# Kernel tuning notes

Measured on AMD Instinct MI355X. Metric: run time of the kernel, lower is better.

The kernel has to match this reference:

```python
import jax, jax.numpy as jnp
import numpy as np

B, C, N, H = 4, 256, 4096, 4
DK = C // H


def _proj(x, w, b):
    # Conv1d with kernel size 1 == per-point linear: [B,C,N] x [O,C] -> [B,O,N]
    return jnp.einsum('oc,bcn->bon', w, x) + b[None, :, None]


def setup_inputs() -> dict:
    key = jax.random.key(0)
    ks = jax.random.split(key, 9)
    s = 1.0 / np.sqrt(C)
    return {
        'x': jax.random.normal(ks[0], (B, C, N), jnp.float32),
        'wq': jax.random.normal(ks[1], (C, C), jnp.float32) * s,
        'bq': jax.random.normal(ks[2], (C,), jnp.float32) * 0.01,
        'wk': jax.random.normal(ks[3], (C, C), jnp.float32) * s,
        'bk': jax.random.normal(ks[4], (C,), jnp.float32) * 0.01,
        'wv': jax.random.normal(ks[5], (C, C), jnp.float32) * s,
        'bv': jax.random.normal(ks[6], (C,), jnp.float32) * 0.01,
        'wp': jax.random.normal(ks[7], (C, C), jnp.float32) * s,
        'bp': jax.random.normal(ks[8], (C,), jnp.float32) * 0.01,
    }


def reference(x, wq, bq, wk, bk, wv, bv, wp, bp):
    b, c, n = x.shape
    q = _proj(x, wq, bq).reshape(b, H, DK, n)
    k = _proj(x, wk, bk).reshape(b, H, DK, n)
    v = _proj(x, wv, bv).reshape(b, H, DK, n)
    scale = 1.0 / jnp.sqrt(jnp.asarray(DK, x.dtype))
    # scores over point pairs: [B,H,N,N]
    scores = jnp.einsum('bhdn,bhdm->bhnm', q, k) * scale
    attn = jax.nn.softmax(scores, axis=-1)
    out = jnp.einsum('bhnm,bhdm->bhdn', attn, v)  # [B,H,DK,N]
    out = out.reshape(b, c, n)
    out = _proj(out, wp, bp)
    return out + x
```

## Files before the change

kernel.cpp:

```cpp
#include <hip/hip_runtime.h>


#define BDIM 4
#define CDIM 256
#define NDIM 4096
#define HDIM 4
#define DKDIM 64
#define QSCALE 0.18033688011112042f

typedef __bf16 bf16x8 __attribute__((ext_vector_type(8)));
typedef float f32x4 __attribute__((ext_vector_type(4)));
typedef short s16x4 __attribute__((ext_vector_type(4)));
typedef unsigned short u16;

__device__ __forceinline__ u16 f2bf(float f) {
  union { __bf16 h; u16 s; } u; u.h = (__bf16)f; return u.s;
}

__global__ __launch_bounds__(256) void wcvt_kernel(
    const float* __restrict__ w0, const float* __restrict__ w1,
    const float* __restrict__ w2, const float* __restrict__ w3,
    u16* __restrict__ d0, u16* __restrict__ d1,
    u16* __restrict__ d2, u16* __restrict__ d3)
{
  const int row = blockIdx.x;
  const int m = blockIdx.y;
  const float* s = (m == 0) ? w0 : (m == 1) ? w1 : (m == 2) ? w2 : w3;
  u16* d = (m == 0) ? d0 : (m == 1) ? d1 : (m == 2) ? d2 : d3;
  const float sc = (m == 0) ? QSCALE : 1.0f;
  const int idx = row * CDIM + threadIdx.x;
  d[idx] = f2bf(s[idx] * sc);
}

__global__ __launch_bounds__(256) void xt_kernel(
    const float* __restrict__ x, u16* __restrict__ xT)
{
  const int b = blockIdx.z, c0 = blockIdx.y * 64, n0 = blockIdx.x * 64;
  __shared__ __align__(16) float T[64][68];
  const int t = threadIdx.x;
  {
    const int cr = t >> 4, nc = (t & 15) * 4;
    #pragma unroll
    for (int ci = 0; ci < 4; ++ci) {
      const float4 v = *(const float4*)&x[((size_t)(b * CDIM + c0 + cr + ci * 16)) * NDIM + n0 + nc];
      *(float4*)&T[cr + ci * 16][nc] = v;
    }
  }
  __syncthreads();
  {
    const int n = t >> 2, g = t & 3;
    union { u16 u[16]; uint4 v[2]; } pk;
    #pragma unroll
    for (int u_ = 0; u_ < 16; ++u_) pk.u[u_] = f2bf(T[g * 16 + u_][n]);
    uint4* dst = (uint4*)&xT[((size_t)(b * NDIM + n0 + n)) * CDIM + c0 + g * 16];
    dst[0] = pk.v[0]; dst[1] = pk.v[1];
  }
}

template<int MODE>
__global__ __launch_bounds__(256, 2) void proj_kernel(
    const u16* __restrict__ xT, const u16* __restrict__ wb,
    const float* __restrict__ bias, const float* __restrict__ res,
    void* __restrict__ outp, float bscale)
{
  const int b = blockIdx.z, o0 = blockIdx.y * 128, n0 = blockIdx.x * 64;
  __shared__ __align__(16) u16 XTs[64][40];
  __shared__ __align__(16) u16 Ws[128][40];
  const int t = threadIdx.x, lane = t & 63, w = t >> 6;
  const int qd = lane >> 4, lm = lane & 15;

  f32x4 acc[4][2];
  #pragma unroll
  for (int nt = 0; nt < 4; ++nt)
    #pragma unroll
    for (int j = 0; j < 2; ++j) acc[nt][j] = (f32x4){0.f, 0.f, 0.f, 0.f};

  for (int cs = 0; cs < 8; ++cs) {
    const int c0 = cs * 32;
    __syncthreads();
    {
      const int r = t >> 2, g = t & 3;
      *(uint4*)&XTs[r][g * 8] =
          *(const uint4*)&xT[((size_t)(b * NDIM + n0 + r)) * CDIM + c0 + g * 8];
      const int r2 = t >> 1, g2 = (t & 1) * 16;
      const u16* wr = &wb[(size_t)(o0 + r2) * CDIM + c0 + g2];
      *(uint4*)&Ws[r2][g2]     = *(const uint4*)(wr);
      *(uint4*)&Ws[r2][g2 + 8] = *(const uint4*)(wr + 8);
    }
    __syncthreads();
    bf16x8 xf[4], wf[2];
    #pragma unroll
    for (int nt = 0; nt < 4; ++nt) xf[nt] = *(const bf16x8*)&XTs[16 * nt + lm][qd * 8];
    #pragma unroll
    for (int j = 0; j < 2; ++j) wf[j] = *(const bf16x8*)&Ws[32 * w + 16 * j + lm][qd * 8];
    #pragma unroll
    for (int nt = 0; nt < 4; ++nt)
      #pragma unroll
      for (int j = 0; j < 2; ++j) {
        if constexpr (MODE == 0)
          acc[nt][j] = __builtin_amdgcn_mfma_f32_16x16x32_bf16(xf[nt], wf[j], acc[nt][j], 0, 0, 0);
        else
          acc[nt][j] = __builtin_amdgcn_mfma_f32_16x16x32_bf16(wf[j], xf[nt], acc[nt][j], 0, 0, 0);
      }
  }

  if constexpr (MODE == 0) {
    u16* out = (u16*)outp;
    #pragma unroll
    for (int j = 0; j < 2; ++j) {
      const int og = o0 + 32 * w + 16 * j + lm;
      const float bv = bias[og] * bscale;
      #pragma unroll
      for (int nt = 0; nt < 4; ++nt)
        #pragma unroll
        for (int r = 0; r < 4; ++r) {
          const int n = n0 + 16 * nt + 4 * qd + r;
          out[((size_t)(b * NDIM + n)) * CDIM + og] = f2bf(acc[nt][j][r] + bv);
        }
    }
  } else {
    #pragma unroll
    for (int j = 0; j < 2; ++j) {
      const float4 b4 = *(const float4*)&bias[o0 + 32 * w + 16 * j + 4 * qd];
      const float bvr[4] = {b4.x, b4.y, b4.z, b4.w};
      #pragma unroll
      for (int nt = 0; nt < 4; ++nt)
        #pragma unroll
        for (int r = 0; r < 4; ++r) {
          const int og = o0 + 32 * w + 16 * j + 4 * qd + r;
          const int n = n0 + 16 * nt + lm;
          const size_t idx = ((size_t)(b * CDIM + og)) * NDIM + n;
          const float val = acc[nt][j][r] + bvr[r];
          if constexpr (MODE == 1) ((u16*)outp)[idx] = f2bf(val);
          else ((float*)outp)[idx] = val + res[idx];
        }
    }
  }
}

__global__ __launch_bounds__(256, 2) void attn_kernel(
    const u16* __restrict__ qT, const u16* __restrict__ kT,
    const u16* __restrict__ vB, u16* __restrict__ abT)
{
  const int bh = blockIdx.y, b = bh >> 2, h = bh & 3;
  const int n0 = blockIdx.x * 128;
  __shared__ __align__(16) u16 Qt[128][72];
  __shared__ __align__(16) u16 Kt[64][72];
  __shared__ __align__(16) u16 Vt[64][72];

  const int t = threadIdx.x, lane = t & 63, w = t >> 6;
  const int qd = lane >> 4, lm = lane & 15;

  {
    const int r = t >> 1, g = (t & 1) * 32;
    const uint4* src = (const uint4*)&qT[((size_t)(b * NDIM + n0 + r)) * CDIM + h * 64 + g];
    uint4* dst = (uint4*)&Qt[r][g];
    dst[0] = src[0]; dst[1] = src[1]; dst[2] = src[2]; dst[3] = src[3];
  }
  __syncthreads();
  bf16x8 qf[2][2];
  #pragma unroll
  for (int s = 0; s < 2; ++s)
    #pragma unroll
    for (int hh = 0; hh < 2; ++hh)
      qf[s][hh] = *(const bf16x8*)&Qt[16 * (2 * w + s) + lm][32 * hh + qd * 8];

  float m_i[2] = {-1e30f, -1e30f}, l_i[2] = {0.f, 0.f};
  f32x4 oa[2][4];
  #pragma unroll
  for (int s = 0; s < 2; ++s)
    #pragma unroll
    for (int dt = 0; dt < 4; ++dt) oa[s][dt] = (f32x4){0.f, 0.f, 0.f, 0.f};

  for (int kt = 0; kt < NDIM; kt += 64) {
    __syncthreads();
    {
      const int r = t >> 2, g = (t & 3) * 16;
      const uint4* ks = (const uint4*)&kT[((size_t)(b * NDIM + kt + r)) * CDIM + h * 64 + g];
      uint4* kd = (uint4*)&Kt[r][g];
      kd[0] = ks[0]; kd[1] = ks[1];
      const uint4* vs = (const uint4*)&vB[((size_t)(b * CDIM + h * 64 + r)) * NDIM + kt + g];
      uint4* vd = (uint4*)&Vt[r][g];
      vd[0] = vs[0]; vd[1] = vs[1];
    }
    __syncthreads();

    bf16x8 kf[4][2];
    #pragma unroll
    for (int nt = 0; nt < 4; ++nt)
      #pragma unroll
      for (int hh = 0; hh < 2; ++hh)
        kf[nt][hh] = *(const bf16x8*)&Kt[16 * nt + lm][32 * hh + qd * 8];

    float pr[2][4][4];
    #pragma unroll
    for (int s = 0; s < 2; ++s) {
      f32x4 sc[4];
      #pragma unroll
      for (int nt = 0; nt < 4; ++nt) {
        f32x4 z = (f32x4){0.f, 0.f, 0.f, 0.f};
        z = __builtin_amdgcn_mfma_f32_16x16x32_bf16(kf[nt][0], qf[s][0], z, 0, 0, 0);
        z = __builtin_amdgcn_mfma_f32_16x16x32_bf16(kf[nt][1], qf[s][1], z, 0, 0, 0);
        sc[nt] = z;
      }
      float mx = sc[0][0];
      #pragma unroll
      for (int nt = 0; nt < 4; ++nt)
        #pragma unroll
        for (int r = 0; r < 4; ++r) mx = fmaxf(mx, sc[nt][r]);
      mx = fmaxf(mx, __shfl_xor(mx, 16));
      mx = fmaxf(mx, __shfl_xor(mx, 32));
      const float mn = fmaxf(m_i[s], mx);
      const float al = __builtin_amdgcn_exp2f(m_i[s] - mn);
      m_i[s] = mn;
      float rs = 0.f;
      #pragma unroll
      for (int nt = 0; nt < 4; ++nt)
        #pragma unroll
        for (int r = 0; r < 4; ++r) {
          const float p = __builtin_amdgcn_exp2f(sc[nt][r] - mn);
          pr[s][nt][r] = p;
          rs += p;
        }
      rs += __shfl_xor(rs, 16);
      rs += __shfl_xor(rs, 32);
      l_i[s] = l_i[s] * al + rs;
      #pragma unroll
      for (int dt = 0; dt < 4; ++dt) oa[s][dt] *= al;
    }

    #pragma unroll
    for (int c = 0; c < 4; ++c) {
      s16x4 av[4];
      #pragma unroll
      for (int dt = 0; dt < 4; ++dt)
        av[dt] = *(const s16x4*)&Vt[16 * dt + lm][16 * c + 4 * qd];
      union { u16 u[4]; s16x4 v; } bp0, bp1;
      #pragma unroll
      for (int r = 0; r < 4; ++r) { bp0.u[r] = f2bf(pr[0][c][r]); bp1.u[r] = f2bf(pr[1][c][r]); }
      #pragma unroll
      for (int dt = 0; dt < 4; ++dt) {
        oa[0][dt] = __builtin_amdgcn_mfma_f32_16x16x16bf16_1k(av[dt], bp0.v, oa[0][dt], 0, 0, 0);
        oa[1][dt] = __builtin_amdgcn_mfma_f32_16x16x16bf16_1k(av[dt], bp1.v, oa[1][dt], 0, 0, 0);
      }
    }
  }

  __syncthreads();
  u16 (*Ot)[72] = (u16(*)[72])&Qt[0][0];
  #pragma unroll
  for (int s = 0; s < 2; ++s) {
    const float inv = 1.0f / l_i[s];
    #pragma unroll
    for (int dt = 0; dt < 4; ++dt)
      #pragma unroll
      for (int r = 0; r < 4; ++r)
        Ot[16 * (2 * w + s) + lm][16 * dt + 4 * qd + r] = f2bf(oa[s][dt][r] * inv);
  }
  __syncthreads();
  {
    const int r = t >> 1, g = (t & 1) * 32;
    uint4* dst = (uint4*)&abT[((size_t)(b * NDIM + n0 + r)) * CDIM + h * 64 + g];
    const uint4* srcp = (const uint4*)&Ot[r][g];
    dst[0] = srcp[0]; dst[1] = srcp[1]; dst[2] = srcp[2]; dst[3] = srcp[3];
  }
}

extern "C" void kernel_launch(void* const* d_in, const int* in_sizes, int n_in,
                              void* d_out, int out_size, void* d_ws, size_t ws_size,
                              hipStream_t stream)
{
  const float* x  = (const float*)d_in[0];
  const float* wq = (const float*)d_in[1];
  const float* bq = (const float*)d_in[2];
  const float* wk = (const float*)d_in[3];
  const float* bk = (const float*)d_in[4];
  const float* wv = (const float*)d_in[5];
  const float* bv = (const float*)d_in[6];
  const float* wp = (const float*)d_in[7];
  const float* bp = (const float*)d_in[8];
  float* out = (float*)d_out;

  const size_t sz = (size_t)BDIM * CDIM * NDIM;
  const size_t wsz = (size_t)CDIM * CDIM;
  u16* xTb = (u16*)d_ws;
  u16* wqb = xTb + sz;
  u16* wkb = wqb + wsz;
  u16* wvb = wkb + wsz;
  u16* wpb = wvb + wsz;
  u16* qTb = wpb + wsz;
  u16* kTb = qTb + sz;
  u16* vBb = kTb + sz;
  u16* abT = vBb + sz;

  const dim3 blk(256);
  wcvt_kernel<<<dim3(CDIM, 4), blk, 0, stream>>>(wq, wk, wv, wp, wqb, wkb, wvb, wpb);
  xt_kernel<<<dim3(NDIM / 64, CDIM / 64, BDIM), blk, 0, stream>>>(x, xTb);
  const dim3 gp(NDIM / 64, 2, BDIM);
  proj_kernel<0><<<gp, blk, 0, stream>>>(xTb, wqb, bq, nullptr, qTb, QSCALE);
  proj_kernel<0><<<gp, blk, 0, stream>>>(xTb, wkb, bk, nullptr, kTb, 1.0f);
  proj_kernel<1><<<gp, blk, 0, stream>>>(xTb, wvb, bv, nullptr, vBb, 1.0f);
  attn_kernel<<<dim3(NDIM / 128, BDIM * HDIM), blk, 0, stream>>>(qTb, kTb, vBb, abT);
  proj_kernel<2><<<gp, blk, 0, stream>>>(abT, wpb, bp, x, out, 1.0f);
}
```

Before: 239.4 us.

## Split attention KV range in two with combine kernel, shrink projection tiles

The attention kernel now divides the key/value sequence into two halves across a third grid dimension. Each half writes a normalized partial output plus its row max and sum, and a new combine kernel merges the two with log-sum-exp weights. This doubles the number of attention blocks (512 → 1024) to fill more CUs, at the cost of extra partial-output traffic and one more launch. The running-max rescale is also skipped when no lane's max increases. Projection kernels use 64-wide output tiles with higher occupancy bounds, which doubles their grid.

```diff
diff --git a/kernel.cpp b/kernel.cpp
--- a/kernel.cpp
+++ b/kernel.cpp
@@ -6,6 +6,7 @@
 #define NDIM 4096
 #define HDIM 4
 #define DKDIM 64
+#define NQ   (BDIM * HDIM * NDIM)
 #define QSCALE 0.18033688011112042f
 
 typedef __bf16 bf16x8 __attribute__((ext_vector_type(8)));
@@ -15,6 +16,9 @@
 
 __device__ __forceinline__ u16 f2bf(float f) {
   union { __bf16 h; u16 s; } u; u.h = (__bf16)f; return u.s;
+}
+__device__ __forceinline__ float bf2f(u16 v) {
+  union { unsigned u; float f; } x; x.u = (unsigned)v << 16; return x.f;
 }
 
 __global__ __launch_bounds__(256) void wcvt_kernel(
@@ -58,92 +62,79 @@
 }
 
 template<int MODE>
-__global__ __launch_bounds__(256, 2) void proj_kernel(
+__global__ __launch_bounds__(256, 4) void proj_kernel(
     const u16* __restrict__ xT, const u16* __restrict__ wb,
     const float* __restrict__ bias, const float* __restrict__ res,
     void* __restrict__ outp, float bscale)
 {
-  const int b = blockIdx.z, o0 = blockIdx.y * 128, n0 = blockIdx.x * 64;
+  const int b = blockIdx.z, o0 = blockIdx.y * 64, n0 = blockIdx.x * 64;
   __shared__ __align__(16) u16 XTs[64][40];
-  __shared__ __align__(16) u16 Ws[128][40];
+  __shared__ __align__(16) u16 Ws[64][40];
   const int t = threadIdx.x, lane = t & 63, w = t >> 6;
   const int qd = lane >> 4, lm = lane & 15;
-
-  f32x4 acc[4][2];
-  #pragma unroll
-  for (int nt = 0; nt < 4; ++nt)
-    #pragma unroll
-    for (int j = 0; j < 2; ++j) acc[nt][j] = (f32x4){0.f, 0.f, 0.f, 0.f};
+  const int sr = t >> 2, sg = (t & 3) * 8;
+
+  const u16* xsrc = xT + ((size_t)(b * NDIM + n0 + sr)) * CDIM + sg;
+  const u16* wsrc = wb + ((size_t)(o0 + sr)) * CDIM + sg;
+
+  f32x4 acc[4];
+  #pragma unroll
+  for (int nt = 0; nt < 4; ++nt) acc[nt] = (f32x4){0.f, 0.f, 0.f, 0.f};
 
   for (int cs = 0; cs < 8; ++cs) {
-    const int c0 = cs * 32;
     __syncthreads();
-    {
-      const int r = t >> 2, g = t & 3;
-      *(uint4*)&XTs[r][g * 8] =
-          *(const uint4*)&xT[((size_t)(b * NDIM + n0 + r)) * CDIM + c0 + g * 8];
-      const int r2 = t >> 1, g2 = (t & 1) * 16;
-      const u16* wr = &wb[(size_t)(o0 + r2) * CDIM + c0 + g2];
-      *(uint4*)&Ws[r2][g2]     = *(const uint4*)(wr);
-      *(uint4*)&Ws[r2][g2 + 8] = *(const uint4*)(wr + 8);
-    }
+    *(uint4*)&XTs[sr][sg] = *(const uint4*)(xsrc + cs * 32);
+    *(uint4*)&Ws[sr][sg]  = *(const uint4*)(wsrc + cs * 32);
     __syncthreads();
-    bf16x8 xf[4], wf[2];
+    bf16x8 xf[4];
     #pragma unroll
     for (int nt = 0; nt < 4; ++nt) xf[nt] = *(const bf16x8*)&XTs[16 * nt + lm][qd * 8];
-    #pragma unroll
-    for (int j = 0; j < 2; ++j) wf[j] = *(const bf16x8*)&Ws[32 * w + 16 * j + lm][qd * 8];
-    #pragma unroll
-    for (int nt = 0; nt < 4; ++nt)
-      #pragma unroll
-      for (int j = 0; j < 2; ++j) {
-        if constexpr (MODE == 0)
-          acc[nt][j] = __builtin_amdgcn_mfma_f32_16x16x32_bf16(xf[nt], wf[j], acc[nt][j], 0, 0, 0);
-        else
-          acc[nt][j] = __builtin_amdgcn_mfma_f32_16x16x32_bf16(wf[j], xf[nt], acc[nt][j], 0, 0, 0);
-      }
+    const bf16x8 wf = *(const bf16x8*)&Ws[16 * w + lm][qd * 8];
+    #pragma unroll
+    for (int nt = 0; nt < 4; ++nt) {
+      if constexpr (MODE == 0)
+        acc[nt] = __builtin_amdgcn_mfma_f32_16x16x32_bf16(xf[nt], wf, acc[nt], 0, 0, 0);
+      else
+        acc[nt] = __builtin_amdgcn_mfma_f32_16x16x32_bf16(wf, xf[nt], acc[nt], 0, 0, 0);
+    }
   }
 
   if constexpr (MODE == 0) {
     u16* out = (u16*)outp;
-    #pragma unroll
-    for (int j = 0; j < 2; ++j) {
-      const int og = o0 + 32 * w + 16 * j + lm;
-      const float bv = bias[og] * bscale;
-      #pragma unroll
-      for (int nt = 0; nt < 4; ++nt)
-        #pragma unroll
-        for (int r = 0; r < 4; ++r) {
-          const int n = n0 + 16 * nt + 4 * qd + r;
-          out[((size_t)(b * NDIM + n)) * CDIM + og] = f2bf(acc[nt][j][r] + bv);
-        }
-    }
+    const int og = o0 + 16 * w + lm;
+    const float bv = bias[og] * bscale;
+    #pragma unroll
+    for (int nt = 0; nt < 4; ++nt)
+      #pragma unroll
+      for (int r = 0; r < 4; ++r) {
+        const int n = n0 + 16 * nt + 4 * qd + r;
+        out[((size_t)(b * NDIM + n)) * CDIM + og] = f2bf(acc[nt][r] + bv);
+      }
   } else {
-    #pragma unroll
-    for (int j = 0; j < 2; ++j) {
-      const float4 b4 = *(const float4*)&bias[o0 + 32 * w + 16 * j + 4 * qd];
-      const float bvr[4] = {b4.x, b4.y, b4.z, b4.w};
-      #pragma unroll
-      for (int nt = 0; nt < 4; ++nt)
-        #pragma unroll
-        for (int r = 0; r < 4; ++r) {
-          const int og = o0 + 32 * w + 16 * j + 4 * qd + r;
-          const int n = n0 + 16 * nt + lm;
-          const size_t idx = ((size_t)(b * CDIM + og)) * NDIM + n;
-          const float val = acc[nt][j][r] + bvr[r];
-          if constexpr (MODE == 1) ((u16*)outp)[idx] = f2bf(val);
-          else ((float*)outp)[idx] = val + res[idx];
-        }
-    }
-  }
-}
-
-__global__ __launch_bounds__(256, 2) void attn_kernel(
+    const float4 b4 = *(const float4*)&bias[o0 + 16 * w + 4 * qd];
+    const float bvr[4] = {b4.x, b4.y, b4.z, b4.w};
+    #pragma unroll
+    for (int nt = 0; nt < 4; ++nt)
+      #pragma unroll
+      for (int r = 0; r < 4; ++r) {
+        const int og = o0 + 16 * w + 4 * qd + r;
+        const int n = n0 + 16 * nt + lm;
+        const size_t idx = ((size_t)(b * CDIM + og)) * NDIM + n;
+        const float val = acc[nt][r] + bvr[r];
+        if constexpr (MODE == 1) ((u16*)outp)[idx] = f2bf(val);
+        else ((float*)outp)[idx] = val + res[idx];
+      }
+  }
+}
+
+__global__ __launch_bounds__(256, 4) void attn_kernel(
     const u16* __restrict__ qT, const u16* __restrict__ kT,
-    const u16* __restrict__ vB, u16* __restrict__ abT)
+    const u16* __restrict__ vB, u16* __restrict__ Opart,
+    float* __restrict__ Mp, float* __restrict__ Lp)
 {
   const int bh = blockIdx.y, b = bh >> 2, h = bh & 3;
   const int n0 = blockIdx.x * 128;
+  const int z  = blockIdx.z;
   __shared__ __align__(16) u16 Qt[128][72];
   __shared__ __align__(16) u16 Kt[64][72];
   __shared__ __align__(16) u16 Vt[64][72];
@@ -172,17 +163,22 @@
     #pragma unroll
     for (int dt = 0; dt < 4; ++dt) oa[s][dt] = (f32x4){0.f, 0.f, 0.f, 0.f};
 
-  for (int kt = 0; kt < NDIM; kt += 64) {
+  const int sr = t >> 2, sg = (t & 3) * 16;
+  const u16* kptr = kT + ((size_t)(b * NDIM) + z * 2048 + sr) * CDIM + h * 64 + sg;
+  const u16* vptr = vB + ((size_t)(b * CDIM) + h * 64 + sr) * NDIM + z * 2048 + sg;
+
+  for (int it = 0; it < 32; ++it) {
     __syncthreads();
     {
-      const int r = t >> 2, g = (t & 3) * 16;
-      const uint4* ks = (const uint4*)&kT[((size_t)(b * NDIM + kt + r)) * CDIM + h * 64 + g];
-      uint4* kd = (uint4*)&Kt[r][g];
-      kd[0] = ks[0]; kd[1] = ks[1];
-      const uint4* vs = (const uint4*)&vB[((size_t)(b * CDIM + h * 64 + r)) * NDIM + kt + g];
-      uint4* vd = (uint4*)&Vt[r][g];
-      vd[0] = vs[0]; vd[1] = vs[1];
-    }
+      uint4* kd = (uint4*)&Kt[sr][sg];
+      kd[0] = *(const uint4*)(kptr);
+      kd[1] = *(const uint4*)(kptr + 8);
+      uint4* vd = (uint4*)&Vt[sr][sg];
+      vd[0] = *(const uint4*)(vptr);
+      vd[1] = *(const uint4*)(vptr + 8);
+    }
+    kptr += (size_t)64 * CDIM;
+    vptr += 64;
     __syncthreads();
 
     bf16x8 kf[4][2];
@@ -198,10 +194,10 @@
       f32x4 sc[4];
       #pragma unroll
       for (int nt = 0; nt < 4; ++nt) {
-        f32x4 z = (f32x4){0.f, 0.f, 0.f, 0.f};
-        z = __builtin_amdgcn_mfma_f32_16x16x32_bf16(kf[nt][0], qf[s][0], z, 0, 0, 0);
-        z = __builtin_amdgcn_mfma_f32_16x16x32_bf16(kf[nt][1], qf[s][1], z, 0, 0, 0);
-        sc[nt] = z;
+        f32x4 zz = (f32x4){0.f, 0.f, 0.f, 0.f};
+        zz = __builtin_amdgcn_mfma_f32_16x16x32_bf16(kf[nt][0], qf[s][0], zz, 0, 0, 0);
+        zz = __builtin_amdgcn_mfma_f32_16x16x32_bf16(kf[nt][1], qf[s][1], zz, 0, 0, 0);
+        sc[nt] = zz;
       }
       float mx = sc[0][0];
       #pragma unroll
@@ -211,7 +207,12 @@
       mx = fmaxf(mx, __shfl_xor(mx, 16));
       mx = fmaxf(mx, __shfl_xor(mx, 32));
       const float mn = fmaxf(m_i[s], mx);
-      const float al = __builtin_amdgcn_exp2f(m_i[s] - mn);
+      if (__any(mx > m_i[s])) {
+        const float al = __builtin_amdgcn_exp2f(m_i[s] - mn);
+        l_i[s] *= al;
+        #pragma unroll
+        for (int dt = 0; dt < 4; ++dt) oa[s][dt] *= al;
+      }
       m_i[s] = mn;
       float rs = 0.f;
       #pragma unroll
@@ -224,9 +225,7 @@
         }
       rs += __shfl_xor(rs, 16);
       rs += __shfl_xor(rs, 32);
-      l_i[s] = l_i[s] * al + rs;
-      #pragma unroll
-      for (int dt = 0; dt < 4; ++dt) oa[s][dt] *= al;
+      l_i[s] += rs;
     }
 
     #pragma unroll
@@ -257,13 +256,53 @@
       for (int r = 0; r < 4; ++r)
         Ot[16 * (2 * w + s) + lm][16 * dt + 4 * qd + r] = f2bf(oa[s][dt][r] * inv);
   }
+  if (qd == 0) {
+    const size_t mlbase = ((size_t)z * (BDIM * HDIM) + bh) * NDIM;
+    #pragma unroll
+    for (int s = 0; s < 2; ++s) {
+      const int q = n0 + 16 * (2 * w + s) + lm;
+      Mp[mlbase + q] = m_i[s];
+      Lp[mlbase + q] = l_i[s];
+    }
+  }
   __syncthreads();
   {
     const int r = t >> 1, g = (t & 1) * 32;
-    uint4* dst = (uint4*)&abT[((size_t)(b * NDIM + n0 + r)) * CDIM + h * 64 + g];
+    u16* dst = Opart + (((size_t)z * (BDIM * HDIM) + bh) * NDIM + n0 + r) * DKDIM + g;
     const uint4* srcp = (const uint4*)&Ot[r][g];
-    dst[0] = srcp[0]; dst[1] = srcp[1]; dst[2] = srcp[2]; dst[3] = srcp[3];
-  }
+    uint4* d4 = (uint4*)dst;
+    d4[0] = srcp[0]; d4[1] = srcp[1]; d4[2] = srcp[2]; d4[3] = srcp[3];
+  }
+}
+
+__global__ __launch_bounds__(256) void combine_kernel(
+    const u16* __restrict__ Opart, const float* __restrict__ Mp,
+    const float* __restrict__ Lp, u16* __restrict__ abT)
+{
+  const int t = threadIdx.x;
+  const int gq = blockIdx.x * 64 + (t >> 2);
+  const int seg = (t & 3) * 16;
+  const float m0 = Mp[gq], l0 = Lp[gq];
+  const float m1 = Mp[NQ + gq], l1 = Lp[NQ + gq];
+  const float M = fmaxf(m0, m1);
+  const float d0 = l0 * __builtin_amdgcn_exp2f(m0 - M);
+  const float d1 = l1 * __builtin_amdgcn_exp2f(m1 - M);
+  const float inv = 1.0f / (d0 + d1);
+  const float w0 = d0 * inv, w1 = d1 * inv;
+
+  const u16* p0 = Opart + (size_t)gq * DKDIM + seg;
+  const u16* p1 = Opart + (size_t)NQ * DKDIM + (size_t)gq * DKDIM + seg;
+  union { u16 u[16]; uint4 v[2]; } a0, a1, ov;
+  a0.v[0] = ((const uint4*)p0)[0]; a0.v[1] = ((const uint4*)p0)[1];
+  a1.v[0] = ((const uint4*)p1)[0]; a1.v[1] = ((const uint4*)p1)[1];
+  #pragma unroll
+  for (int j = 0; j < 16; ++j)
+    ov.u[j] = f2bf(w0 * bf2f(a0.u[j]) + w1 * bf2f(a1.u[j]));
+
+  const int bh = gq >> 12, n = gq & (NDIM - 1);
+  const int b = bh >> 2, h = bh & 3;
+  uint4* dst = (uint4*)&abT[((size_t)(b * NDIM + n)) * CDIM + h * 64 + seg];
+  dst[0] = ov.v[0]; dst[1] = ov.v[1];
 }
 
 extern "C" void kernel_launch(void* const* d_in, const int* in_sizes, int n_in,
@@ -281,7 +320,7 @@
   const float* bp = (const float*)d_in[8];
   float* out = (float*)d_out;
 
-  const size_t sz = (size_t)BDIM * CDIM * NDIM;
+  const size_t sz  = (size_t)BDIM * CDIM * NDIM;
   const size_t wsz = (size_t)CDIM * CDIM;
   u16* xTb = (u16*)d_ws;
   u16* wqb = xTb + sz;
@@ -292,14 +331,18 @@
   u16* kTb = qTb + sz;
   u16* vBb = kTb + sz;
   u16* abT = vBb + sz;
+  u16* Opart = abT + sz;
+  float* Mp = (float*)(Opart + 2 * sz);
+  float* Lp = Mp + 2 * (size_t)NQ;
 
   const dim3 blk(256);
   wcvt_kernel<<<dim3(CDIM, 4), blk, 0, stream>>>(wq, wk, wv, wp, wqb, wkb, wvb, wpb);
   xt_kernel<<<dim3(NDIM / 64, CDIM / 64, BDIM), blk, 0, stream>>>(x, xTb);
-  const dim3 gp(NDIM / 64, 2, BDIM);
+  const dim3 gp(NDIM / 64, 4, BDIM);
   proj_kernel<0><<<gp, blk, 0, stream>>>(xTb, wqb, bq, nullptr, qTb, QSCALE);
   proj_kernel<0><<<gp, blk, 0, stream>>>(xTb, wkb, bk, nullptr, kTb, 1.0f);
   proj_kernel<1><<<gp, blk, 0, stream>>>(xTb, wvb, bv, nullptr, vBb, 1.0f);
-  attn_kernel<<<dim3(NDIM / 128, BDIM * HDIM), blk, 0, stream>>>(qTb, kTb, vBb, abT);
+  attn_kernel<<<dim3(NDIM / 128, BDIM * HDIM, 2), blk, 0, stream>>>(qTb, kTb, vBb, Opart, Mp, Lp);
+  combine_kernel<<<dim3(NQ / 64), blk, 0, stream>>>(Opart, Mp, Lp, abT);
   proj_kernel<2><<<gp, blk, 0, stream>>>(abT, wpb, bp, x, out, 1.0f);
 }
```

New measurement: 232.0 us. -3.1%, faster.
